# Performance work log

Measured on AMD Instinct MI355X. Metric: run time of the kernel, lower is better.

## Reference

```python
import jax, jax.numpy as jnp
import numpy as np

IN_FEATURES = 256
OUT_FEATURES = 64
ALPHA = 0.2  # leaky relu slope


def _xavier_uniform(key, shape, gain=1.414):
    fan_in, fan_out = shape[0], shape[1]
    limit = gain * np.sqrt(6.0 / (fan_in + fan_out))
    return jax.random.uniform(key, shape, jnp.float32, -limit, limit)


def setup_inputs() -> dict:
    key = jax.random.key(0)
    k_h, k_W, k_a = jax.random.split(key, 3)
    h = jax.random.normal(k_h, (8, 2048, IN_FEATURES), dtype=jnp.float32)
    W = _xavier_uniform(k_W, (IN_FEATURES, OUT_FEATURES))
    a = _xavier_uniform(k_a, (2 * OUT_FEATURES, 1))
    return {"h": h, "W": W, "a": a}


def reference(h, W, a):
    # h: [B, N, F_in], W: [F_in, D], a: [2D, 1]
    Wh = h @ W  # [B, N, D]
    D = Wh.shape[-1]
    a1 = a[:D, 0]   # attends to source node i (repeat_interleave side)
    a2 = a[D:, 0]   # attends to target node j (repeat side)
    f1 = Wh @ a1    # [B, N]
    f2 = Wh @ a2    # [B, N]
    # e[b, i, j] = leakyrelu(a1.Wh[b,i] + a2.Wh[b,j])  -- identical math to
    # the original's O(N^2 * 2D) repeat/concat, without materializing it.
    e = jax.nn.leaky_relu(f1[:, :, None] + f2[:, None, :], negative_slope=ALPHA)  # [B, N, N]
    # NOTE: original applies softmax over dim=1 (over i, per column j).
    attention = jax.nn.softmax(e, axis=1)  # [B, N, N]
    # dropout is identity in eval mode
    h_prime = jnp.einsum('bij,bjd->bid', attention, Wh)  # [B, N, D]
    return jax.nn.elu(h_prime)  # concat=True path
```

## Files before the change

### kernel.cpp

```cpp
#include <hip/hip_runtime.h>

#define B 8
#define N 2048
#define KF 256
#define DF 64
#define LOG2E 1.44269504088896340736f
#define IC 8
#define ICH (N / IC)

typedef __attribute__((ext_vector_type(8))) short short8;
typedef __attribute__((ext_vector_type(4))) float float4v;

__device__ __forceinline__ float fexp2(float x) {
#if __has_builtin(__builtin_amdgcn_exp2f)
    return __builtin_amdgcn_exp2f(x);
#else
    return exp2f(x);
#endif
}
__device__ __forceinline__ float eluf(float x) {
    return x > 0.f ? x : fexp2(x * LOG2E) - 1.0f;
}
__device__ __forceinline__ short bf16r(float x) {
    unsigned u = __float_as_uint(x);
    return (short)((u + 0x8000u) >> 16);
}
__device__ __forceinline__ unsigned pkbf16(float x, float y) {
#if __has_builtin(__builtin_amdgcn_cvt_pk_bf16_f32)
    auto r = __builtin_amdgcn_cvt_pk_bf16_f32(x, y);
    return *(unsigned*)&r;
#else
    unsigned ux = (__float_as_uint(x) + 0x8000u) >> 16;
    unsigned uy = (__float_as_uint(y) + 0x8000u) & 0xffff0000u;
    return ux | uy;
#endif
}
#define DOT4(c, u, p) \
    p = fmaf(c.x, u.x, fmaf(c.y, u.y, fmaf(c.z, u.z, fmaf(c.w, u.w, p))));

__global__ __launch_bounds__(256) void k_wh(const float* __restrict__ h,
                                            const float* __restrict__ W,
                                            const float* __restrict__ a,
                                            short* __restrict__ WhT,
                                            float* __restrict__ f1,
                                            float* __restrict__ f2) {
    __shared__ __align__(16) unsigned char smem[34816];
    short* lwt  = (short*)smem;
    float* lv   = (float*)(smem + 32768);
    float* lred = (float*)smem;
    float* lp   = (float*)(smem + 16896);

    int t = threadIdx.x;
    int wv = t >> 6, lane = t & 63;
    int n15 = lane & 15, q = lane >> 4;
    int bx = blockIdx.x;

    const float* hr = h + ((long)bx * 32 + n15) * KF + wv * 64 + q * 8;
    float4 c0 = *(const float4*)(hr);
    float4 c1 = *(const float4*)(hr + 4);
    float4 c2 = *(const float4*)(hr + 32);
    float4 c3 = *(const float4*)(hr + 36);

    {
        const float4* wr4 = (const float4*)(W + t * DF);
        float s1 = 0.f, s2 = 0.f;
        #pragma unroll
        for (int c = 0; c < 16; c++) {
            float4 w4 = wr4[c];
            float4 a1v = *(const float4*)(a + 4 * c);
            float4 a2v = *(const float4*)(a + DF + 4 * c);
            lwt[(4 * c + 0) * 256 + t] = bf16r(w4.x);
            lwt[(4 * c + 1) * 256 + t] = bf16r(w4.y);
            lwt[(4 * c + 2) * 256 + t] = bf16r(w4.z);
            lwt[(4 * c + 3) * 256 + t] = bf16r(w4.w);
            s1 = fmaf(w4.x, a1v.x, fmaf(w4.y, a1v.y, fmaf(w4.z, a1v.z, fmaf(w4.w, a1v.w, s1))));
            s2 = fmaf(w4.x, a2v.x, fmaf(w4.y, a2v.y, fmaf(w4.z, a2v.z, fmaf(w4.w, a2v.w, s2))));
        }
        lv[t] = s1;
        lv[256 + t] = s2;
    }
    __syncthreads();

    const short* bq = lwt + n15 * 256 + wv * 64 + q * 8;
    short8 s0b0 = *(const short8*)(bq);
    short8 s0b1 = *(const short8*)(bq + 16 * 256);
    short8 s0b2 = *(const short8*)(bq + 32 * 256);
    short8 s0b3 = *(const short8*)(bq + 48 * 256);
    short8 s1b0 = *(const short8*)(bq + 32);
    short8 s1b1 = *(const short8*)(bq + 16 * 256 + 32);
    short8 s1b2 = *(const short8*)(bq + 32 * 256 + 32);
    short8 s1b3 = *(const short8*)(bq + 48 * 256 + 32);
    const float* vv = lv + wv * 64 + q * 8;
    float4 u00 = *(const float4*)(vv);
    float4 u01 = *(const float4*)(vv + 4);
    float4 u10 = *(const float4*)(vv + 32);
    float4 u11 = *(const float4*)(vv + 36);
    float4 x00 = *(const float4*)(vv + 256);
    float4 x01 = *(const float4*)(vv + 256 + 4);
    float4 x10 = *(const float4*)(vv + 256 + 32);
    float4 x11 = *(const float4*)(vv + 256 + 36);
    __syncthreads();

    #pragma unroll
    for (int rt = 0; rt < 2; rt++) {
        float4 m0, m1, m2, m3;
        if (rt < 1) {
            const float* hn = hr + 16 * KF;
            m0 = *(const float4*)(hn);
            m1 = *(const float4*)(hn + 4);
            m2 = *(const float4*)(hn + 32);
            m3 = *(const float4*)(hn + 36);
        }
        float p1 = 0.f, p2 = 0.f;
        DOT4(c0, u00, p1) DOT4(c1, u01, p1) DOT4(c2, u10, p1) DOT4(c3, u11, p1)
        DOT4(c0, x00, p2) DOT4(c1, x01, p2) DOT4(c2, x10, p2) DOT4(c3, x11, p2)

        short8 af0 = { bf16r(c0.x), bf16r(c0.y), bf16r(c0.z), bf16r(c0.w),
                       bf16r(c1.x), bf16r(c1.y), bf16r(c1.z), bf16r(c1.w) };
        short8 af1 = { bf16r(c2.x), bf16r(c2.y), bf16r(c2.z), bf16r(c2.w),
                       bf16r(c3.x), bf16r(c3.y), bf16r(c3.z), bf16r(c3.w) };
        float4v acc0 = {0.f, 0.f, 0.f, 0.f}, acc1 = acc0, acc2 = acc0, acc3 = acc0;
        acc0 = __builtin_amdgcn_mfma_f32_16x16x32_bf16(af0, s0b0, acc0, 0, 0, 0);
        acc0 = __builtin_amdgcn_mfma_f32_16x16x32_bf16(af1, s1b0, acc0, 0, 0, 0);
        acc1 = __builtin_amdgcn_mfma_f32_16x16x32_bf16(af0, s0b1, acc1, 0, 0, 0);
        acc1 = __builtin_amdgcn_mfma_f32_16x16x32_bf16(af1, s1b1, acc1, 0, 0, 0);
        acc2 = __builtin_amdgcn_mfma_f32_16x16x32_bf16(af0, s0b2, acc2, 0, 0, 0);
        acc2 = __builtin_amdgcn_mfma_f32_16x16x32_bf16(af1, s1b2, acc2, 0, 0, 0);
        acc3 = __builtin_amdgcn_mfma_f32_16x16x32_bf16(af0, s0b3, acc3, 0, 0, 0);
        acc3 = __builtin_amdgcn_mfma_f32_16x16x32_bf16(af1, s1b3, acc3, 0, 0, 0);

        #define STASH(nb, A)                                                  \
            {                                                                 \
                _Pragma("unroll")                                             \
                for (int r = 0; r < 4; r++)                                   \
                    lred[wv * 1056 + (q * 4 + r) * 66 + nb * 16 + n15] = A[r]; \
            }
        STASH(0, acc0) STASH(1, acc1) STASH(2, acc2) STASH(3, acc3)
        #undef STASH
        p1 += __shfl_xor(p1, 16, 64); p1 += __shfl_xor(p1, 32, 64);
        p2 += __shfl_xor(p2, 16, 64); p2 += __shfl_xor(p2, 32, 64);
        if (q == 0) { lp[wv * 16 + n15] = p1; lp[64 + wv * 16 + n15] = p2; }
        __syncthreads();

        long i0 = (long)bx * 32 + rt * 16;
        int d = t & 63, ig = t >> 6;
        int bb = (int)(i0 >> 11);
        int il = (int)(i0 & (N - 1));
        float s0 = 0.f, s1 = 0.f, s2 = 0.f, s3 = 0.f;
        #pragma unroll
        for (int w = 0; w < 4; w++) {
            const float* lr = lred + w * 1056 + (ig * 4) * 66 + d;
            s0 += lr[0]; s1 += lr[66]; s2 += lr[132]; s3 += lr[198];
        }
        short4 pk = make_short4(bf16r(s0), bf16r(s1), bf16r(s2), bf16r(s3));
        int jj = il + ig * 4;
        *(short4*)(WhT + (((long)bb * 32 + (jj >> 6)) * 64 + d) * 64 + (jj & 63)) = pk;

        if (t < 16) {
            f1[i0 + t] = lp[t] + lp[16 + t] + lp[32 + t] + lp[48 + t];
        } else if (t < 32) {
            int tt = t + 48;
            f2[i0 + t - 16] = lp[tt] + lp[16 + tt] + lp[32 + tt] + lp[48 + tt];
        }
        __syncthreads();
        c0 = m0; c1 = m1; c2 = m2; c3 = m3;
    }
}

__global__ __launch_bounds__(256) void k_denom(const float* __restrict__ f1,
                                               const float* __restrict__ f2,
                                               float* __restrict__ dpart) {
    __shared__ float2 le[ICH];
    int t = threadIdx.x;
    int b = blockIdx.z, ic = blockIdx.y;
    int j = blockIdx.x * 256 + t;
    float v = f1[b * N + ic * ICH + t];
    le[t] = make_float2(fexp2(v * LOG2E), fexp2(v * 0.2f * LOG2E));
    __syncthreads();
    float f2j = f2[b * N + j];
    float E2  = fexp2(f2j * LOG2E);
    float E2s = fexp2(f2j * 0.2f * LOG2E);
    float s = 0.f;
    const float4* le4 = (const float4*)le;
    for (int ii = 0; ii < ICH / 2; ii++) {
        float4 u = le4[ii];
        s += fmaxf(u.x * E2, u.y * E2s);
        s += fmaxf(u.z * E2, u.w * E2s);
    }
    dpart[((long)ic * B + b) * N + j] = s;
}

__global__ __launch_bounds__(512) void k_attn(const short* __restrict__ WhT,
                                              const float* __restrict__ f1,
                                              const float* __restrict__ f2,
                                              const float* __restrict__ dpart,
                                              float* __restrict__ out) {
    __shared__ __align__(16) unsigned char smem[40960];
    int t = threadIdx.x;
    int wv = t >> 6, lane = t & 63;
    int g = wv >> 1, wg = wv & 1, lt2 = t & 127;
    int n15 = lane & 15, q = lane >> 4;
    int it = blockIdx.x, b = blockIdx.y;
    int i0 = it * 64 + wg * 32;

    float f1a = f1[b * N + i0 + n15];
    float f1b = f1[b * N + i0 + 16 + n15];
    float E1a = fexp2(f1a * LOG2E),  E1sa = fexp2(f1a * 0.2f * LOG2E);
    float E1b = fexp2(f1b * LOG2E),  E1sb = fexp2(f1b * 0.2f * LOG2E);

    uint4*  ls = (uint4*)smem + g * 576;
    float2* lc = (float2*)(smem + 36864) + g * 128;
    const uint4* wsrc = (const uint4*)WhT + ((long)b * 32 + g * 8) * 512;
    const float* f2b = f2 + b * N + g * 512;
    const float* dpb = dpart + b * N + g * 512;

    uint4 r0, r1, r2, r3;
    float pf2, pd0, pd1, pd2, pd3, pd4, pd5, pd6, pd7;

    #define LOADC(cc) {                                     \
        const uint4* gp = wsrc + (cc) * 512;                \
        r0 = gp[lt2];       r1 = gp[128 + lt2];             \
        r2 = gp[256 + lt2]; r3 = gp[384 + lt2];             \
    }
    #define LOADP(cc) {                                     \
        if (lt2 < 64) {                                     \
            int jb2 = (cc) * 64 + lt2;                      \
            pf2 = f2b[jb2];                                 \
            pd0 = dpb[jb2];              pd1 = dpb[16384 + jb2]; \
            pd2 = dpb[2 * 16384 + jb2];  pd3 = dpb[3 * 16384 + jb2]; \
            pd4 = dpb[4 * 16384 + jb2];  pd5 = dpb[5 * 16384 + jb2]; \
            pd6 = dpb[6 * 16384 + jb2];  pd7 = dpb[7 * 16384 + jb2]; \
        }                                                   \
    }
    #define STOREC() {                                      \
        int rb = lt2 >> 3, cl = lt2 & 7;                    \
        ls[rb * 9 + cl] = r0;        ls[(16 + rb) * 9 + cl] = r1; \
        ls[(32 + rb) * 9 + cl] = r2; ls[(48 + rb) * 9 + cl] = r3; \
    }
    #define LCC(buf) {                                      \
        if (lt2 < 64) {                                     \
            float den = ((pd0 + pd1) + (pd2 + pd3)) + ((pd4 + pd5) + (pd6 + pd7)); \
            float rr = 1.0f / den;                          \
            float E2  = fexp2(pf2 * LOG2E);                 \
            float E2s = fexp2(pf2 * 0.2f * LOG2E);          \
            lc[(buf) * 64 + lt2] = make_float2(E2 * rr, E2s * rr); \
        }                                                   \
    }

    LOADC(0) LOADP(0)
    STOREC() LCC(0)
    __syncthreads();

    float4v accA0 = {0.f, 0.f, 0.f, 0.f}, accA1 = accA0, accA2 = accA0, accA3 = accA0;
    float4v accB0 = accA0, accB1 = accA0, accB2 = accA0, accB3 = accA0;

    for (int c = 0; c < 8; c++) {
        int cur = c & 1;
        if (c < 7) { LOADC(c + 1) LOADP(c + 1) }

        const short* lsS = (const short*)ls;
        const float4* lcf = (const float4*)(lc + cur * 64);
        #pragma unroll
        for (int js = 0; js < 2; js++) {
            const float4* cp4 = lcf + js * 16 + q * 4;
            float4 p01 = cp4[0], p23 = cp4[1], p45 = cp4[2], p67 = cp4[3];
            float A0 = fmaxf(E1a * p01.x, E1sa * p01.y);
            float A1 = fmaxf(E1a * p01.z, E1sa * p01.w);
            float A2 = fmaxf(E1a * p23.x, E1sa * p23.y);
            float A3 = fmaxf(E1a * p23.z, E1sa * p23.w);
            float A4 = fmaxf(E1a * p45.x, E1sa * p45.y);
            float A5 = fmaxf(E1a * p45.z, E1sa * p45.w);
            float A6 = fmaxf(E1a * p67.x, E1sa * p67.y);
            float A7 = fmaxf(E1a * p67.z, E1sa * p67.w);
            float B0 = fmaxf(E1b * p01.x, E1sb * p01.y);
            float B1 = fmaxf(E1b * p01.z, E1sb * p01.w);
            float B2 = fmaxf(E1b * p23.x, E1sb * p23.y);
            float B3 = fmaxf(E1b * p23.z, E1sb * p23.w);
            float B4 = fmaxf(E1b * p45.x, E1sb * p45.y);
            float B5 = fmaxf(E1b * p45.z, E1sb * p45.w);
            float B6 = fmaxf(E1b * p67.x, E1sb * p67.y);
            float B7 = fmaxf(E1b * p67.z, E1sb * p67.w);
            uint4 ua = { pkbf16(A0, A1), pkbf16(A2, A3), pkbf16(A4, A5), pkbf16(A6, A7) };
            uint4 ub = { pkbf16(B0, B1), pkbf16(B2, B3), pkbf16(B4, B5), pkbf16(B6, B7) };
            short8 afA = *(short8*)&ua;
            short8 afB = *(short8*)&ub;

            const short* bp = lsS + js * 32 + q * 8;
            short8 b0 = *(const short8*)(bp + (n15 +  0) * 72);
            short8 b1 = *(const short8*)(bp + (n15 + 16) * 72);
            short8 b2 = *(const short8*)(bp + (n15 + 32) * 72);
            short8 b3 = *(const short8*)(bp + (n15 + 48) * 72);

            accA0 = __builtin_amdgcn_mfma_f32_16x16x32_bf16(afA, b0, accA0, 0, 0, 0);
            accA1 = __builtin_amdgcn_mfma_f32_16x16x32_bf16(afA, b1, accA1, 0, 0, 0);
            accA2 = __builtin_amdgcn_mfma_f32_16x16x32_bf16(afA, b2, accA2, 0, 0, 0);
            accA3 = __builtin_amdgcn_mfma_f32_16x16x32_bf16(afA, b3, accA3, 0, 0, 0);
            accB0 = __builtin_amdgcn_mfma_f32_16x16x32_bf16(afB, b0, accB0, 0, 0, 0);
            accB1 = __builtin_amdgcn_mfma_f32_16x16x32_bf16(afB, b1, accB1, 0, 0, 0);
            accB2 = __builtin_amdgcn_mfma_f32_16x16x32_bf16(afB, b2, accB2, 0, 0, 0);
            accB3 = __builtin_amdgcn_mfma_f32_16x16x32_bf16(afB, b3, accB3, 0, 0, 0);
        }

        if (c < 7) {
            __syncthreads();
            STOREC() LCC((c + 1) & 1)
            __syncthreads();
        }
    }
    #undef LOADC
    #undef LOADP
    #undef STOREC
    #undef LCC

    float* epi = (float*)smem;
    int row_o = t >> 3, d0 = (t & 7) * 8;
    int wg_o = row_o >> 5, r31 = row_o & 31;
    const float* e1p = epi + wg_o * 2176 + r31 * 68 + d0;
    const float* e2p = epi + (2 + wg_o) * 2176 + r31 * 68 + d0;

    #define ESTASH(rg) {                                                     \
        float* ep = epi + (rg) * 2176 + (q * 4) * 68 + n15;                  \
        _Pragma("unroll")                                                    \
        for (int r = 0; r < 4; r++) {                                        \
            ep[r * 68 +  0] = accA0[r]; ep[r * 68 + 16] = accA1[r];          \
            ep[r * 68 + 32] = accA2[r]; ep[r * 68 + 48] = accA3[r];          \
            ep[(16 * 68) + r * 68 +  0] = accB0[r];                          \
            ep[(16 * 68) + r * 68 + 16] = accB1[r];                          \
            ep[(16 * 68) + r * 68 + 32] = accB2[r];                          \
            ep[(16 * 68) + r * 68 + 48] = accB3[r];                          \
        }                                                                    \
    }

    __syncthreads();
    if (g < 2) ESTASH(wv)
    __syncthreads();
    float4 sa0 = *(const float4*)(e1p);
    float4 sa1 = *(const float4*)(e1p + 4);
    float4 sb0 = *(const float4*)(e2p);
    float4 sb1 = *(const float4*)(e2p + 4);
    float4 t0, t1;
    t0.x = sa0.x + sb0.x; t0.y = sa0.y + sb0.y; t0.z = sa0.z + sb0.z; t0.w = sa0.w + sb0.w;
    t1.x = sa1.x + sb1.x; t1.y = sa1.y + sb1.y; t1.z = sa1.z + sb1.z; t1.w = sa1.w + sb1.w;
    __syncthreads();
    if (g >= 2) ESTASH(wv - 4)
    __syncthreads();
    #undef ESTASH
    float4 ua0 = *(const float4*)(e1p);
    float4 ua1 = *(const float4*)(e1p + 4);
    float4 ub0 = *(const float4*)(e2p);
    float4 ub1 = *(const float4*)(e2p + 4);
    float4 o0, o1;
    o0.x = eluf(t0.x + ua0.x + ub0.x); o0.y = eluf(t0.y + ua0.y + ub0.y);
    o0.z = eluf(t0.z + ua0.z + ub0.z); o0.w = eluf(t0.w + ua0.w + ub0.w);
    o1.x = eluf(t1.x + ua1.x + ub1.x); o1.y = eluf(t1.y + ua1.y + ub1.y);
    o1.z = eluf(t1.z + ua1.z + ub1.z); o1.w = eluf(t1.w + ua1.w + ub1.w);
    float* op = out + ((long)b * N + it * 64 + row_o) * DF + d0;
    *(float4*)(op) = o0;
    *(float4*)(op + 4) = o1;
}

extern "C" void kernel_launch(void* const* d_in, const int* in_sizes, int n_in,
                              void* d_out, int out_size, void* d_ws, size_t ws_size,
                              hipStream_t stream) {
    const float* h = (const float*)d_in[0];
    const float* W = (const float*)d_in[1];
    const float* a = (const float*)d_in[2];
    float* out = (float*)d_out;

    char* ws = (char*)d_ws;
    const size_t NB = (size_t)B * N;
    size_t off = 0;
    short* WhT   = (short*)(ws + off); off += NB * DF * sizeof(short);
    float* f1    = (float*)(ws + off); off += NB * sizeof(float);
    float* f2    = (float*)(ws + off); off += NB * sizeof(float);
    float* dpart = (float*)(ws + off); off += (size_t)IC * NB * sizeof(float);
    (void)off; (void)ws_size;

    k_wh<<<NB / 32, 256, 0, stream>>>(h, W, a, WhT, f1, f2);
    k_denom<<<dim3(N / 256, IC, B), 256, 0, stream>>>(f1, f2, dpart);
    k_attn<<<dim3(N / 64, B), 512, 0, stream>>>(WhT, f1, f2, dpart, out);
}
```

Before: 91.55 us.

## Replace quadratic attention with sort-based prefix-sum formulation

Leaky ReLU is piecewise linear in f1[i]+f2[j], so exp(e) factors as E1*E2 or E1s*E2s depending on the sign of the sum. The new code sorts f2 and f1 per batch with a bitonic sort, builds prefix sums over the sorted order to get each column's softmax denominator, and builds prefix sums of the weighted Wh rows. Each output row then becomes a binary-search index plus two lookups, which removes the O(N^2) denominator and MFMA attention passes. In exchange it adds a serial bitonic sort and scans in a tiny grid (4x8 blocks of 1024 threads), runs in fp32 with long prefix sums that may lose precision, and replaces the bf16 MFMA work.

```diff
diff --git a/kernel.cpp b/kernel.cpp
--- a/kernel.cpp
+++ b/kernel.cpp
@@ -5,8 +5,7 @@
 #define KF 256
 #define DF 64
 #define LOG2E 1.44269504088896340736f
-#define IC 8
-#define ICH (N / IC)
+#define NR 2049
 
 typedef __attribute__((ext_vector_type(8))) short short8;
 typedef __attribute__((ext_vector_type(4))) float float4v;
@@ -25,23 +24,13 @@
     unsigned u = __float_as_uint(x);
     return (short)((u + 0x8000u) >> 16);
 }
-__device__ __forceinline__ unsigned pkbf16(float x, float y) {
-#if __has_builtin(__builtin_amdgcn_cvt_pk_bf16_f32)
-    auto r = __builtin_amdgcn_cvt_pk_bf16_f32(x, y);
-    return *(unsigned*)&r;
-#else
-    unsigned ux = (__float_as_uint(x) + 0x8000u) >> 16;
-    unsigned uy = (__float_as_uint(y) + 0x8000u) & 0xffff0000u;
-    return ux | uy;
-#endif
-}
 #define DOT4(c, u, p) \
     p = fmaf(c.x, u.x, fmaf(c.y, u.y, fmaf(c.z, u.z, fmaf(c.w, u.w, p))));
 
 __global__ __launch_bounds__(256) void k_wh(const float* __restrict__ h,
                                             const float* __restrict__ W,
                                             const float* __restrict__ a,
-                                            short* __restrict__ WhT,
+                                            float* __restrict__ Wh,
                                             float* __restrict__ f1,
                                             float* __restrict__ f2) {
     __shared__ __align__(16) unsigned char smem[34816];
@@ -152,9 +141,11 @@
             const float* lr = lred + w * 1056 + (ig * 4) * 66 + d;
             s0 += lr[0]; s1 += lr[66]; s2 += lr[132]; s3 += lr[198];
         }
-        short4 pk = make_short4(bf16r(s0), bf16r(s1), bf16r(s2), bf16r(s3));
-        int jj = il + ig * 4;
-        *(short4*)(WhT + (((long)bb * 32 + (jj >> 6)) * 64 + d) * 64 + (jj & 63)) = pk;
+        float* wp = Wh + ((long)bb * N + il + ig * 4) * DF + d;
+        wp[0]      = s0;
+        wp[DF]     = s1;
+        wp[2 * DF] = s2;
+        wp[3 * DF] = s3;
 
         if (t < 16) {
             f1[i0 + t] = lp[t] + lp[16 + t] + lp[32 + t] + lp[48 + t];
@@ -167,196 +158,151 @@
     }
 }
 
-__global__ __launch_bounds__(256) void k_denom(const float* __restrict__ f1,
+__global__ __launch_bounds__(1024) void k_prep(const float* __restrict__ Wh,
+                                               const float* __restrict__ f1,
                                                const float* __restrict__ f2,
-                                               float* __restrict__ dpart) {
-    __shared__ float2 le[ICH];
+                                               int* __restrict__ tIdx,
+                                               float* __restrict__ SSg,
+                                               float* __restrict__ PSgs) {
+    __shared__ float sv[2048];
+    __shared__ int   si[2048];
+    __shared__ float gA[2048];
+    __shared__ float gsA[2048];
+    __shared__ __align__(16) unsigned char un[25088];
+    float* f1s  = (float*)un;
+    float* ps1  = (float*)(un + 8192);
+    float* ps1s = (float*)(un + 16640);
+    float* sG   = (float*)un;
+    float* sGs  = (float*)(un + 4096);
+
     int t = threadIdx.x;
-    int b = blockIdx.z, ic = blockIdx.y;
-    int j = blockIdx.x * 256 + t;
-    float v = f1[b * N + ic * ICH + t];
-    le[t] = make_float2(fexp2(v * LOG2E), fexp2(v * 0.2f * LOG2E));
-    __syncthreads();
-    float f2j = f2[b * N + j];
-    float E2  = fexp2(f2j * LOG2E);
-    float E2s = fexp2(f2j * 0.2f * LOG2E);
-    float s = 0.f;
-    const float4* le4 = (const float4*)le;
-    for (int ii = 0; ii < ICH / 2; ii++) {
-        float4 u = le4[ii];
-        s += fmaxf(u.x * E2, u.y * E2s);
-        s += fmaxf(u.z * E2, u.w * E2s);
-    }
-    dpart[((long)ic * B + b) * N + j] = s;
-}
-
-__global__ __launch_bounds__(512) void k_attn(const short* __restrict__ WhT,
-                                              const float* __restrict__ f1,
-                                              const float* __restrict__ f2,
-                                              const float* __restrict__ dpart,
-                                              float* __restrict__ out) {
-    __shared__ __align__(16) unsigned char smem[40960];
+    int dsl = blockIdx.x, b = blockIdx.y;
+    const float* f1g = f1 + b * N;
+    const float* f2g = f2 + b * N;
+
+    sv[t] = f2g[t];  sv[t + 1024] = f2g[t + 1024];
+    si[t] = t;       si[t + 1024] = t + 1024;
+    f1s[t] = f1g[t]; f1s[t + 1024] = f1g[t + 1024];
+    __syncthreads();
+
+    for (int k = 2; k <= 2048; k <<= 1) {
+        for (int j = k >> 1; j > 0; j >>= 1) {
+            int i1 = ((t & ~(j - 1)) << 1) | (t & (j - 1));
+            int i2 = i1 | j;
+            bool up = (i1 & k) == 0;
+            float a  = sv[i1],  c  = sv[i2];
+            int   ia = si[i1],  ic = si[i2];
+            if ((a > c) == up) { sv[i1] = c; sv[i2] = a; si[i1] = ic; si[i2] = ia; }
+            float fa = f1s[i1], fc = f1s[i2];
+            if ((fa > fc) == up) { f1s[i1] = fc; f1s[i2] = fa; }
+            __syncthreads();
+        }
+    }
+
+    if (t < 64) {
+        float a1 = 0.f, a2 = 0.f;
+        #pragma unroll 4
+        for (int x = 0; x < 32; x++) {
+            float v = f1s[t * 32 + x];
+            a1 += fexp2(v * LOG2E);
+            a2 += fexp2(v * 0.2f * LOG2E);
+        }
+        gA[t] = a1; gsA[t] = a2;
+    }
+    __syncthreads();
+    if (t < 64) {
+        float o1 = 0.f, o2 = 0.f;
+        for (int s = 0; s < t; s++) { o1 += gA[s]; o2 += gsA[s]; }
+        for (int x = 0; x < 32; x++) {
+            int p = t * 32 + x;
+            ps1[p] = o1; ps1s[p] = o2;
+            float v = f1s[p];
+            o1 += fexp2(v * LOG2E);
+            o2 += fexp2(v * 0.2f * LOG2E);
+        }
+        if (t == 63) { ps1[2048] = o1; ps1s[2048] = o2; }
+    }
+    __syncthreads();
+
+    float tot1 = ps1[2048], tot1s = ps1s[2048];
+    for (int p = t; p < 2048; p += 1024) {
+        float v   = sv[p];
+        float E2  = fexp2(v * LOG2E);
+        float E2s = fexp2(v * 0.2f * LOG2E);
+        float key = -v;
+        int lo = 0, hi = 2048;
+        while (lo < hi) { int mid = (lo + hi) >> 1; if (f1s[mid] < key) lo = mid + 1; else hi = mid; }
+        float den = E2 * (tot1 - ps1[lo]) + E2s * ps1s[lo];
+        float rr = 1.0f / den;
+        gA[p] = E2 * rr; gsA[p] = E2s * rr;
+    }
+    if (dsl == 0) {
+        for (int i = t; i < 2048; i += 1024) {
+            float key = -f1g[i];
+            int lo = 0, hi = 2048;
+            while (lo < hi) { int mid = (lo + hi) >> 1; if (sv[mid] < key) lo = mid + 1; else hi = mid; }
+            tIdx[b * N + i] = lo;
+        }
+    }
+    __syncthreads();
+
+    int seg = t >> 4, dl = t & 15;
+    int d = dsl * 16 + dl;
+    const float* whb = Wh + (((long)b) << 11) * DF;
+    float w[32];
+    float ag = 0.f, ags = 0.f;
+    #pragma unroll
+    for (int x = 0; x < 32; x++) {
+        int p = seg * 32 + x;
+        float wv = whb[si[p] * DF + d];
+        w[x] = wv;
+        ag  += gA[p] * wv;
+        ags += gsA[p] * wv;
+    }
+    sG[seg * 16 + dl] = ag; sGs[seg * 16 + dl] = ags;
+    __syncthreads();
+    float og = 0.f, ogs = 0.f, tot = 0.f, tots = 0.f;
+    for (int s = 0; s < 64; s++) {
+        float vg = sG[s * 16 + dl], vgs = sGs[s * 16 + dl];
+        if (s < seg) { og += vg; ogs += vgs; }
+        tot += vg; tots += vgs;
+    }
+    (void)tots;
+    float* pg  = SSg  + ((long)b * NR) * DF + d;
+    float* pgs = PSgs + ((long)b * NR) * DF + d;
+    #pragma unroll
+    for (int x = 0; x < 32; x++) {
+        int p = seg * 32 + x;
+        pg [(long)p * DF] = tot - og;
+        pgs[(long)p * DF] = ogs;
+        og  += gA[p]  * w[x];
+        ogs += gsA[p] * w[x];
+    }
+    if (seg == 63) { pg[2048L * DF] = tot - og; pgs[2048L * DF] = ogs; }
+}
+
+__global__ __launch_bounds__(256) void k_out(const float* __restrict__ f1,
+                                             const int* __restrict__ tIdx,
+                                             const float* __restrict__ SSg,
+                                             const float* __restrict__ PSgs,
+                                             float* __restrict__ out) {
     int t = threadIdx.x;
-    int wv = t >> 6, lane = t & 63;
-    int g = wv >> 1, wg = wv & 1, lt2 = t & 127;
-    int n15 = lane & 15, q = lane >> 4;
-    int it = blockIdx.x, b = blockIdx.y;
-    int i0 = it * 64 + wg * 32;
-
-    float f1a = f1[b * N + i0 + n15];
-    float f1b = f1[b * N + i0 + 16 + n15];
-    float E1a = fexp2(f1a * LOG2E),  E1sa = fexp2(f1a * 0.2f * LOG2E);
-    float E1b = fexp2(f1b * LOG2E),  E1sb = fexp2(f1b * 0.2f * LOG2E);
-
-    uint4*  ls = (uint4*)smem + g * 576;
-    float2* lc = (float2*)(smem + 36864) + g * 128;
-    const uint4* wsrc = (const uint4*)WhT + ((long)b * 32 + g * 8) * 512;
-    const float* f2b = f2 + b * N + g * 512;
-    const float* dpb = dpart + b * N + g * 512;
-
-    uint4 r0, r1, r2, r3;
-    float pf2, pd0, pd1, pd2, pd3, pd4, pd5, pd6, pd7;
-
-    #define LOADC(cc) {                                     \
-        const uint4* gp = wsrc + (cc) * 512;                \
-        r0 = gp[lt2];       r1 = gp[128 + lt2];             \
-        r2 = gp[256 + lt2]; r3 = gp[384 + lt2];             \
-    }
-    #define LOADP(cc) {                                     \
-        if (lt2 < 64) {                                     \
-            int jb2 = (cc) * 64 + lt2;                      \
-            pf2 = f2b[jb2];                                 \
-            pd0 = dpb[jb2];              pd1 = dpb[16384 + jb2]; \
-            pd2 = dpb[2 * 16384 + jb2];  pd3 = dpb[3 * 16384 + jb2]; \
-            pd4 = dpb[4 * 16384 + jb2];  pd5 = dpb[5 * 16384 + jb2]; \
-            pd6 = dpb[6 * 16384 + jb2];  pd7 = dpb[7 * 16384 + jb2]; \
-        }                                                   \
-    }
-    #define STOREC() {                                      \
-        int rb = lt2 >> 3, cl = lt2 & 7;                    \
-        ls[rb * 9 + cl] = r0;        ls[(16 + rb) * 9 + cl] = r1; \
-        ls[(32 + rb) * 9 + cl] = r2; ls[(48 + rb) * 9 + cl] = r3; \
-    }
-    #define LCC(buf) {                                      \
-        if (lt2 < 64) {                                     \
-            float den = ((pd0 + pd1) + (pd2 + pd3)) + ((pd4 + pd5) + (pd6 + pd7)); \
-            float rr = 1.0f / den;                          \
-            float E2  = fexp2(pf2 * LOG2E);                 \
-            float E2s = fexp2(pf2 * 0.2f * LOG2E);          \
-            lc[(buf) * 64 + lt2] = make_float2(E2 * rr, E2s * rr); \
-        }                                                   \
-    }
-
-    LOADC(0) LOADP(0)
-    STOREC() LCC(0)
-    __syncthreads();
-
-    float4v accA0 = {0.f, 0.f, 0.f, 0.f}, accA1 = accA0, accA2 = accA0, accA3 = accA0;
-    float4v accB0 = accA0, accB1 = accA0, accB2 = accA0, accB3 = accA0;
-
-    for (int c = 0; c < 8; c++) {
-        int cur = c & 1;
-        if (c < 7) { LOADC(c + 1) LOADP(c + 1) }
-
-        const short* lsS = (const short*)ls;
-        const float4* lcf = (const float4*)(lc + cur * 64);
-        #pragma unroll
-        for (int js = 0; js < 2; js++) {
-            const float4* cp4 = lcf + js * 16 + q * 4;
-            float4 p01 = cp4[0], p23 = cp4[1], p45 = cp4[2], p67 = cp4[3];
-            float A0 = fmaxf(E1a * p01.x, E1sa * p01.y);
-            float A1 = fmaxf(E1a * p01.z, E1sa * p01.w);
-            float A2 = fmaxf(E1a * p23.x, E1sa * p23.y);
-            float A3 = fmaxf(E1a * p23.z, E1sa * p23.w);
-            float A4 = fmaxf(E1a * p45.x, E1sa * p45.y);
-            float A5 = fmaxf(E1a * p45.z, E1sa * p45.w);
-            float A6 = fmaxf(E1a * p67.x, E1sa * p67.y);
-            float A7 = fmaxf(E1a * p67.z, E1sa * p67.w);
-            float B0 = fmaxf(E1b * p01.x, E1sb * p01.y);
-            float B1 = fmaxf(E1b * p01.z, E1sb * p01.w);
-            float B2 = fmaxf(E1b * p23.x, E1sb * p23.y);
-            float B3 = fmaxf(E1b * p23.z, E1sb * p23.w);
-            float B4 = fmaxf(E1b * p45.x, E1sb * p45.y);
-            float B5 = fmaxf(E1b * p45.z, E1sb * p45.w);
-            float B6 = fmaxf(E1b * p67.x, E1sb * p67.y);
-            float B7 = fmaxf(E1b * p67.z, E1sb * p67.w);
-            uint4 ua = { pkbf16(A0, A1), pkbf16(A2, A3), pkbf16(A4, A5), pkbf16(A6, A7) };
-            uint4 ub = { pkbf16(B0, B1), pkbf16(B2, B3), pkbf16(B4, B5), pkbf16(B6, B7) };
-            short8 afA = *(short8*)&ua;
-            short8 afB = *(short8*)&ub;
-
-            const short* bp = lsS + js * 32 + q * 8;
-            short8 b0 = *(const short8*)(bp + (n15 +  0) * 72);
-            short8 b1 = *(const short8*)(bp + (n15 + 16) * 72);
-            short8 b2 = *(const short8*)(bp + (n15 + 32) * 72);
-            short8 b3 = *(const short8*)(bp + (n15 + 48) * 72);
-
-            accA0 = __builtin_amdgcn_mfma_f32_16x16x32_bf16(afA, b0, accA0, 0, 0, 0);
-            accA1 = __builtin_amdgcn_mfma_f32_16x16x32_bf16(afA, b1, accA1, 0, 0, 0);
-            accA2 = __builtin_amdgcn_mfma_f32_16x16x32_bf16(afA, b2, accA2, 0, 0, 0);
-            accA3 = __builtin_amdgcn_mfma_f32_16x16x32_bf16(afA, b3, accA3, 0, 0, 0);
-            accB0 = __builtin_amdgcn_mfma_f32_16x16x32_bf16(afB, b0, accB0, 0, 0, 0);
-            accB1 = __builtin_amdgcn_mfma_f32_16x16x32_bf16(afB, b1, accB1, 0, 0, 0);
-            accB2 = __builtin_amdgcn_mfma_f32_16x16x32_bf16(afB, b2, accB2, 0, 0, 0);
-            accB3 = __builtin_amdgcn_mfma_f32_16x16x32_bf16(afB, b3, accB3, 0, 0, 0);
-        }
-
-        if (c < 7) {
-            __syncthreads();
-            STOREC() LCC((c + 1) & 1)
-            __syncthreads();
-        }
-    }
-    #undef LOADC
-    #undef LOADP
-    #undef STOREC
-    #undef LCC
-
-    float* epi = (float*)smem;
-    int row_o = t >> 3, d0 = (t & 7) * 8;
-    int wg_o = row_o >> 5, r31 = row_o & 31;
-    const float* e1p = epi + wg_o * 2176 + r31 * 68 + d0;
-    const float* e2p = epi + (2 + wg_o) * 2176 + r31 * 68 + d0;
-
-    #define ESTASH(rg) {                                                     \
-        float* ep = epi + (rg) * 2176 + (q * 4) * 68 + n15;                  \
-        _Pragma("unroll")                                                    \
-        for (int r = 0; r < 4; r++) {                                        \
-            ep[r * 68 +  0] = accA0[r]; ep[r * 68 + 16] = accA1[r];          \
-            ep[r * 68 + 32] = accA2[r]; ep[r * 68 + 48] = accA3[r];          \
-            ep[(16 * 68) + r * 68 +  0] = accB0[r];                          \
-            ep[(16 * 68) + r * 68 + 16] = accB1[r];                          \
-            ep[(16 * 68) + r * 68 + 32] = accB2[r];                          \
-            ep[(16 * 68) + r * 68 + 48] = accB3[r];                          \
-        }                                                                    \
-    }
-
-    __syncthreads();
-    if (g < 2) ESTASH(wv)
-    __syncthreads();
-    float4 sa0 = *(const float4*)(e1p);
-    float4 sa1 = *(const float4*)(e1p + 4);
-    float4 sb0 = *(const float4*)(e2p);
-    float4 sb1 = *(const float4*)(e2p + 4);
-    float4 t0, t1;
-    t0.x = sa0.x + sb0.x; t0.y = sa0.y + sb0.y; t0.z = sa0.z + sb0.z; t0.w = sa0.w + sb0.w;
-    t1.x = sa1.x + sb1.x; t1.y = sa1.y + sb1.y; t1.z = sa1.z + sb1.z; t1.w = sa1.w + sb1.w;
-    __syncthreads();
-    if (g >= 2) ESTASH(wv - 4)
-    __syncthreads();
-    #undef ESTASH
-    float4 ua0 = *(const float4*)(e1p);
-    float4 ua1 = *(const float4*)(e1p + 4);
-    float4 ub0 = *(const float4*)(e2p);
-    float4 ub1 = *(const float4*)(e2p + 4);
-    float4 o0, o1;
-    o0.x = eluf(t0.x + ua0.x + ub0.x); o0.y = eluf(t0.y + ua0.y + ub0.y);
-    o0.z = eluf(t0.z + ua0.z + ub0.z); o0.w = eluf(t0.w + ua0.w + ub0.w);
-    o1.x = eluf(t1.x + ua1.x + ub1.x); o1.y = eluf(t1.y + ua1.y + ub1.y);
-    o1.z = eluf(t1.z + ua1.z + ub1.z); o1.w = eluf(t1.w + ua1.w + ub1.w);
-    float* op = out + ((long)b * N + it * 64 + row_o) * DF + d0;
-    *(float4*)(op) = o0;
-    *(float4*)(op + 4) = o1;
+    int b = blockIdx.y;
+    int i0 = blockIdx.x * 64;
+    int rr = t >> 6, d = t & 63;
+    const float* sgB = SSg  + ((long)b * NR) * DF + d;
+    const float* pgB = PSgs + ((long)b * NR) * DF + d;
+    float* ob = out + ((long)b * N + i0) * DF + d;
+    #pragma unroll
+    for (int kk = 0; kk < 16; kk++) {
+        int r = rr + kk * 4;
+        int ti = tIdx[b * N + i0 + r];
+        float v = f1[b * N + i0 + r];
+        float e1  = fexp2(v * LOG2E);
+        float e1s = fexp2(v * 0.2f * LOG2E);
+        float x = e1 * sgB[(long)ti * DF] + e1s * pgB[(long)ti * DF];
+        ob[(long)r * DF] = eluf(x);
+    }
 }
 
 extern "C" void kernel_launch(void* const* d_in, const int* in_sizes, int n_in,
@@ -370,13 +316,15 @@
     char* ws = (char*)d_ws;
     const size_t NB = (size_t)B * N;
     size_t off = 0;
-    short* WhT   = (short*)(ws + off); off += NB * DF * sizeof(short);
-    float* f1    = (float*)(ws + off); off += NB * sizeof(float);
-    float* f2    = (float*)(ws + off); off += NB * sizeof(float);
-    float* dpart = (float*)(ws + off); off += (size_t)IC * NB * sizeof(float);
+    float* Wh   = (float*)(ws + off); off += NB * DF * sizeof(float);
+    float* f1   = (float*)(ws + off); off += NB * sizeof(float);
+    float* f2   = (float*)(ws + off); off += NB * sizeof(float);
+    int*   tIdx = (int*)  (ws + off); off += NB * sizeof(int);
+    float* SSg  = (float*)(ws + off); off += (size_t)B * NR * DF * sizeof(float);
+    float* PSgs = (float*)(ws + off); off += (size_t)B * NR * DF * sizeof(float);
     (void)off; (void)ws_size;
 
-    k_wh<<<NB / 32, 256, 0, stream>>>(h, W, a, WhT, f1, f2);
-    k_denom<<<dim3(N / 256, IC, B), 256, 0, stream>>>(f1, f2, dpart);
-    k_attn<<<dim3(N / 64, B), 512, 0, stream>>>(WhT, f1, f2, dpart, out);
-}
+    k_wh<<<NB / 32, 256, 0, stream>>>(h, W, a, Wh, f1, f2);
+    k_prep<<<dim3(4, B), 1024, 0, stream>>>(Wh, f1, f2, tIdx, SSg, PSgs);
+    k_out<<<dim3(N / 64, B), 256, 0, stream>>>(f1, tIdx, SSg, PSgs, out);
+}
```

Result: slower. 125.6 us (+37.2%).
